# Kernel optimization log

Measured on AMD Instinct MI355X. Metric: run time of the kernel, lower is better.

Reference implementation:

```python
import jax, jax.numpy as jnp
import numpy as np

N_EMBD = 512
NUM_HEADS = 8
HEAD_SIZE = 64


def setup_inputs() -> dict:
    key = jax.random.key(0)
    ks = jax.random.split(key, 6)
    B, T, C, H, D = 64, 256, N_EMBD, NUM_HEADS, HEAD_SIZE
    s = 0.02
    return {
        "x": jax.random.normal(ks[0], (B, T, C), dtype=jnp.float32),
        "wq": jax.random.normal(ks[1], (H, C, D), dtype=jnp.float32) * s,
        "wk": jax.random.normal(ks[2], (H, C, D), dtype=jnp.float32) * s,
        "wv": jax.random.normal(ks[3], (H, C, D), dtype=jnp.float32) * s,
        "bq": jnp.zeros((H, D), dtype=jnp.float32),
        "bk": jnp.zeros((H, D), dtype=jnp.float32),
        "bv": jnp.zeros((H, D), dtype=jnp.float32),
        "wo": jax.random.normal(ks[4], (H * D, C), dtype=jnp.float32) * s,
        "bo": jnp.zeros((C,), dtype=jnp.float32),
    }


def reference(x, wq, wk, wv, bq, bk, bv, wo, bo):
    B, T, C = x.shape
    H, _, D = wq.shape
    # per-head QKV projections (vectorized over heads)
    q = jnp.einsum('btc,hcd->bhtd', x, wq) + bq[None, :, None, :]
    k = jnp.einsum('btc,hcd->bhtd', x, wk) + bk[None, :, None, :]
    v = jnp.einsum('btc,hcd->bhtd', x, wv) + bv[None, :, None, :]
    scale = 1.0 / jnp.sqrt(jnp.asarray(D, dtype=x.dtype))
    scores = jnp.einsum('bhtd,bhsd->bhts', q, k) * scale  # [B,H,T,T]
    causal = jnp.tril(jnp.ones((T, T), dtype=bool))
    scores = jnp.where(causal[None, None], scores, -jnp.inf)
    weights = jax.nn.softmax(scores, axis=-1)  # dropout omitted (eval mode)
    out = jnp.einsum('bhts,bhsd->bhtd', weights, v)  # [B,H,T,D]
    combined = out.transpose(0, 2, 1, 3).reshape(B, T, H * D)
    return combined @ wo + bo
```

## Files before the change

### kernel.cpp

```cpp
#include <hip/hip_runtime.h>

typedef unsigned int   u32;
typedef unsigned short u16;
typedef __attribute__((ext_vector_type(8))) short short8;
typedef __attribute__((ext_vector_type(4))) float f32x4;


__device__ __forceinline__ u16 f2bf(float f) {
    u32 u = __float_as_uint(f);
    u += 0x7fffu + ((u >> 16) & 1u);
    return (u16)(u >> 16);
}

__global__ void cast_x_kernel(const float* __restrict__ x, u16* __restrict__ xb) {
    int i = blockIdx.x * 256 + threadIdx.x;
    float4 v = ((const float4*)x)[i];
    ushort4 o;
    o.x = f2bf(v.x); o.y = f2bf(v.y); o.z = f2bf(v.z); o.w = f2bf(v.w);
    ((ushort4*)xb)[i] = o;
}

__global__ void pack_wqkv_kernel(const float* __restrict__ wq, const float* __restrict__ wk,
                                 const float* __restrict__ wv, u16* __restrict__ wt) {
    int i = blockIdx.x * 256 + threadIdx.x;
    int n = i >> 9, c = i & 511;
    int proj = n >> 9, hd = n & 511;
    int h = hd >> 6, d = hd & 63;
    const float* w = (proj == 0) ? wq : (proj == 1) ? wk : wv;
    wt[(size_t)n * 512 + c] = f2bf(w[h * 32768 + c * 64 + d]);
}

__global__ void pack_wo_kernel(const float* __restrict__ wo, u16* __restrict__ wt) {
    int i = blockIdx.x * 256 + threadIdx.x;
    int n = i >> 9, k = i & 511;
    wt[(size_t)n * 512 + k] = f2bf(wo[(size_t)k * 512 + n]);
}

template<int EPI>
__global__ __launch_bounds__(256)
void gemm128_kernel(const u16* __restrict__ A, const u16* __restrict__ Bt,
                    float* __restrict__ outf, const float* __restrict__ bo,
                    u16* __restrict__ Qb, u16* __restrict__ Kb, u16* __restrict__ Vb,
                    const float* __restrict__ bq, const float* __restrict__ bk,
                    const float* __restrict__ bv) {
    __shared__ __align__(16) u16 As[128 * 40];
    __shared__ __align__(16) u16 Bs[128 * 40];
    const int tid = threadIdx.x;
    const int m0 = blockIdx.y * 128;
    const int n0 = blockIdx.x * 128;
    const int r0 = tid >> 2;
    const int seg = tid & 3;
    const uint4* Ag = (const uint4*)(A + (size_t)m0 * 512);
    const uint4* Bg = (const uint4*)(Bt + (size_t)n0 * 512);
    uint4* AsV = (uint4*)As;
    uint4* BsV = (uint4*)Bs;

    uint4 a0 = Ag[r0 * 64 + seg], a1 = Ag[(r0 + 64) * 64 + seg];
    uint4 b0 = Bg[r0 * 64 + seg], b1 = Bg[(r0 + 64) * 64 + seg];

    const int w = tid >> 6, lane = tid & 63;
    const int wrow = (w >> 1) * 64, wcol = (w & 1) * 64;
    const int lm = lane & 15, quad = lane >> 4;

    f32x4 acc[4][4] = {};

    for (int kt = 0; kt < 16; ++kt) {
        __syncthreads();
        AsV[r0 * 5 + seg] = a0;  AsV[(r0 + 64) * 5 + seg] = a1;
        BsV[r0 * 5 + seg] = b0;  BsV[(r0 + 64) * 5 + seg] = b1;
        __syncthreads();
        if (kt < 15) {
            int ko = (kt + 1) * 4 + seg;
            a0 = Ag[r0 * 64 + ko]; a1 = Ag[(r0 + 64) * 64 + ko];
            b0 = Bg[r0 * 64 + ko]; b1 = Bg[(r0 + 64) * 64 + ko];
        }
        short8 af[4], bf[4];
        #pragma unroll
        for (int mi = 0; mi < 4; ++mi)
            af[mi] = *(const short8*)(As + (wrow + mi * 16 + lm) * 40 + quad * 8);
        #pragma unroll
        for (int ni = 0; ni < 4; ++ni)
            bf[ni] = *(const short8*)(Bs + (wcol + ni * 16 + lm) * 40 + quad * 8);
        #pragma unroll
        for (int mi = 0; mi < 4; ++mi)
            #pragma unroll
            for (int ni = 0; ni < 4; ++ni)
                acc[mi][ni] = __builtin_amdgcn_mfma_f32_16x16x32_bf16(af[mi], bf[ni], acc[mi][ni], 0, 0, 0);
    }

    if (EPI == 1) {
        #pragma unroll
        for (int ni = 0; ni < 4; ++ni) {
            int ncol = n0 + wcol + ni * 16 + lm;
            float bias = bo[ncol];
            #pragma unroll
            for (int mi = 0; mi < 4; ++mi) {
                int mbase = m0 + wrow + mi * 16 + quad * 4;
                #pragma unroll
                for (int r = 0; r < 4; ++r)
                    outf[(size_t)(mbase + r) * 512 + ncol] = acc[mi][ni][r] + bias;
            }
        }
    } else {
        #pragma unroll
        for (int ni = 0; ni < 4; ++ni) {
            int ncol = n0 + wcol + ni * 16 + lm;
            int proj = ncol >> 9, hd = ncol & 511;
            int h = hd >> 6, d = hd & 63;
            const float* bptr = (proj == 0) ? bq : (proj == 1) ? bk : bv;
            u16* dst = (proj == 0) ? Qb : (proj == 1) ? Kb : Vb;
            float bias = bptr[hd];
            #pragma unroll
            for (int mi = 0; mi < 4; ++mi) {
                int mbase = m0 + wrow + mi * 16 + quad * 4;
                #pragma unroll
                for (int r = 0; r < 4; ++r) {
                    int mrow = mbase + r;
                    int b = mrow >> 8, t = mrow & 255;
                    size_t idx = (proj == 2)
                        ? ((size_t)((b * 8 + h) * 64 + d) * 256 + t)
                        : ((size_t)((b * 8 + h) * 256 + t) * 64 + d);
                    dst[idx] = f2bf(acc[mi][ni][r] + bias);
                }
            }
        }
    }
}

__global__ __launch_bounds__(256)
void attn_mfma_kernel(const u16* __restrict__ Qg, const u16* __restrict__ Kg,
                      const u16* __restrict__ Vtg, u16* __restrict__ attn) {
    __shared__ __align__(16) u16 lds[36864];
    const int head = blockIdx.x;
    const int b = head >> 3, h = head & 7;
    const int tid = threadIdx.x;
    const size_t hb = (size_t)head * 16384;

    {
        const uint4* Ksrc = (const uint4*)(Kg + hb);
        const uint4* Vsrc = (const uint4*)(Vtg + hb);
        uint4* L4 = (uint4*)lds;
        #pragma unroll
        for (int it = 0; it < 8; ++it) {
            int g = it * 256 + tid;
            int kr = g >> 3, kc = g & 7;
            L4[kr * 8 + (kc ^ (kr & 7))] = Ksrc[g];
            int vr = g >> 5, vc = g & 31;
            L4[2048 + vr * 32 + (vc ^ (vr & 7))] = Vsrc[g];
        }
    }
    __syncthreads();

    const int w = tid >> 6, lane = tid & 63;
    const int lm = lane & 15, quad = lane >> 4;
    const int l7 = lm & 7;

    const int kx0 = (quad ^ l7) * 8;
    const int kx1 = ((4 + quad) ^ l7) * 8;
    const u16* Kbase = lds + lm * 64;
    const u16* Vbase = lds + 16384 + lm * 256;
    const int Pbase = 32768 + w * 1024;
    const int x0 = (lm >> 3) & 1;
    const int pw_even = Pbase + quad * 16 + l7 + x0 * 8;
    const int pw_odd  = Pbase + quad * 16 + l7 + (x0 ^ 1) * 8;
    const int pr0 = Pbase + ((lm & 3) * 4 + (quad >> 1)) * 64
                  + (2 * (lm >> 2) + ((quad & 1) ^ (lm & 1))) * 8;

    #pragma unroll 1
    for (int i = 0; i < 4; ++i) {
        const int t0 = i * 64 + w * 16;
        short8 qa0 = *(const short8*)(Qg + hb + (size_t)(t0 + lm) * 64 + quad * 8);
        short8 qa1 = *(const short8*)(Qg + hb + (size_t)(t0 + lm) * 64 + 32 + quad * 8);
        f32x4 O[4] = {};
        float mr[4] = {-INFINITY, -INFINITY, -INFINITY, -INFINITY};
        float lr[4] = {0.f, 0.f, 0.f, 0.f};

        #pragma unroll 1
        for (int j = 0; j <= i; ++j) {
            f32x4 S[4] = {};
            #pragma unroll
            for (int ni = 0; ni < 4; ++ni) {
                const u16* kp = Kbase + j * 4096 + ni * 1024;
                short8 kb0 = *(const short8*)(kp + kx0);
                short8 kb1 = *(const short8*)(kp + kx1);
                S[ni] = __builtin_amdgcn_mfma_f32_16x16x32_bf16(qa0, kb0, S[ni], 0, 0, 0);
                S[ni] = __builtin_amdgcn_mfma_f32_16x16x32_bf16(qa1, kb1, S[ni], 0, 0, 0);
            }
            if (j == i) {
                #pragma unroll
                for (int ni = 0; ni < 4; ++ni) {
                    int scol = ni * 16 + lm;
                    #pragma unroll
                    for (int rr = 0; rr < 4; ++rr) {
                        int tloc = w * 16 + quad * 4 + rr;
                        S[ni][rr] = (scol > tloc) ? -INFINITY : S[ni][rr] * 0.125f;
                    }
                }
            } else {
                #pragma unroll
                for (int ni = 0; ni < 4; ++ni)
                    #pragma unroll
                    for (int rr = 0; rr < 4; ++rr)
                        S[ni][rr] *= 0.125f;
            }
            float alpha[4];
            #pragma unroll
            for (int rr = 0; rr < 4; ++rr) {
                float mx = fmaxf(fmaxf(S[0][rr], S[1][rr]), fmaxf(S[2][rr], S[3][rr]));
                mx = fmaxf(mx, __shfl_xor(mx, 1));
                mx = fmaxf(mx, __shfl_xor(mx, 2));
                mx = fmaxf(mx, __shfl_xor(mx, 4));
                mx = fmaxf(mx, __shfl_xor(mx, 8));
                float mnew = fmaxf(mr[rr], mx);
                alpha[rr] = __expf(mr[rr] - mnew);
                mr[rr] = mnew;
            }
            __syncthreads();
            float rs[4] = {0.f, 0.f, 0.f, 0.f};
            #pragma unroll
            for (int ni = 0; ni < 4; ++ni) {
                #pragma unroll
                for (int rr = 0; rr < 4; ++rr) {
                    float p = __expf(S[ni][rr] - mr[rr]);
                    rs[rr] += p;
                    int addr = ((rr & 1) ? pw_odd : pw_even) + (rr * 4 + ni) * 64;
                    lds[addr] = f2bf(p);
                }
            }
            #pragma unroll
            for (int rr = 0; rr < 4; ++rr) {
                float s = rs[rr];
                s += __shfl_xor(s, 1);
                s += __shfl_xor(s, 2);
                s += __shfl_xor(s, 4);
                s += __shfl_xor(s, 8);
                lr[rr] = lr[rr] * alpha[rr] + s;
                O[0][rr] *= alpha[rr]; O[1][rr] *= alpha[rr];
                O[2][rr] *= alpha[rr]; O[3][rr] *= alpha[rr];
            }
            __syncthreads();
            short8 pa0 = *(const short8*)(lds + pr0);
            short8 pa1 = *(const short8*)(lds + pr0 + 128);
            #pragma unroll
            for (int nd = 0; nd < 4; ++nd) {
                const u16* vp = Vbase + nd * 4096 + j * 64;
                short8 vb0 = *(const short8*)(vp + kx0);
                short8 vb1 = *(const short8*)(vp + kx1);
                O[nd] = __builtin_amdgcn_mfma_f32_16x16x32_bf16(pa0, vb0, O[nd], 0, 0, 0);
                O[nd] = __builtin_amdgcn_mfma_f32_16x16x32_bf16(pa1, vb1, O[nd], 0, 0, 0);
            }
        }
        #pragma unroll
        for (int rr = 0; rr < 4; ++rr) {
            float inv = 1.0f / lr[rr];
            int t = t0 + quad * 4 + rr;
            u16* op = attn + (size_t)(b * 256 + t) * 512 + h * 64 + lm;
            op[0]  = f2bf(O[0][rr] * inv);
            op[16] = f2bf(O[1][rr] * inv);
            op[32] = f2bf(O[2][rr] * inv);
            op[48] = f2bf(O[3][rr] * inv);
        }
    }
}

extern "C" void kernel_launch(void* const* d_in, const int* in_sizes, int n_in,
                              void* d_out, int out_size, void* d_ws, size_t ws_size,
                              hipStream_t stream) {
    const float* x  = (const float*)d_in[0];
    const float* wq = (const float*)d_in[1];
    const float* wk = (const float*)d_in[2];
    const float* wv = (const float*)d_in[3];
    const float* bq = (const float*)d_in[4];
    const float* bk = (const float*)d_in[5];
    const float* bv = (const float*)d_in[6];
    const float* wo = (const float*)d_in[7];
    const float* bo = (const float*)d_in[8];
    float* out = (float*)d_out;

    char* ws = (char*)d_ws;
    const size_t SZ = 16777216;
    u16* xb    = (u16*)(ws);
    u16* Qb    = (u16*)(ws + SZ);
    u16* Kb    = (u16*)(ws + 2 * SZ);
    u16* Vt    = (u16*)(ws + 3 * SZ);
    u16* attn  = (u16*)(ws + 4 * SZ);
    u16* wqkvT = (u16*)(ws + 5 * SZ);
    u16* woT   = (u16*)(ws + 5 * SZ + 1572864);

    cast_x_kernel<<<8192, 256, 0, stream>>>(x, xb);
    pack_wqkv_kernel<<<3072, 256, 0, stream>>>(wq, wk, wv, wqkvT);
    pack_wo_kernel<<<1024, 256, 0, stream>>>(wo, woT);

    gemm128_kernel<0><<<dim3(12, 128), 256, 0, stream>>>(
        xb, wqkvT, nullptr, nullptr, Qb, Kb, Vt, bq, bk, bv);

    attn_mfma_kernel<<<512, 256, 0, stream>>>(Qb, Kb, Vt, attn);

    gemm128_kernel<1><<<dim3(4, 128), 256, 0, stream>>>(
        attn, woT, out, bo, nullptr, nullptr, nullptr, nullptr, nullptr, nullptr);
}
```

Measured before the change: 216.8 us.

## Split causal attention across two blocks per head and use direct global-to-LDS loads

The attention kernel now launches two blocks per head, each handling a balanced pair of causal query tiles, (0,3) or (1,2). This doubles the grid for better CU occupancy and load balance, at the cost of each block reloading the full K/V into LDS. The GEMM kernels replace the register-staged prefetch with global_load_lds builtins that write straight into unpadded LDS tiles. That removes VGPR staging but also removes the overlap of next-tile loads with MFMA work, and the unpadded stride may bring back LDS bank conflicts.

```diff
diff --git a/kernel.cpp b/kernel.cpp
--- a/kernel.cpp
+++ b/kernel.cpp
@@ -10,6 +10,12 @@
     u32 u = __float_as_uint(f);
     u += 0x7fffu + ((u >> 16) & 1u);
     return (u16)(u >> 16);
+}
+
+__device__ __forceinline__ void gload_lds16(const u16* g, u16* l) {
+    __builtin_amdgcn_global_load_lds(
+        (const __attribute__((address_space(1))) u32*)(const void*)g,
+        (__attribute__((address_space(3))) u32*)(void*)l, 16, 0, 0);
 }
 
 __global__ void cast_x_kernel(const float* __restrict__ x, u16* __restrict__ xb) {
@@ -43,20 +49,17 @@
                     u16* __restrict__ Qb, u16* __restrict__ Kb, u16* __restrict__ Vb,
                     const float* __restrict__ bq, const float* __restrict__ bk,
                     const float* __restrict__ bv) {
-    __shared__ __align__(16) u16 As[128 * 40];
-    __shared__ __align__(16) u16 Bs[128 * 40];
+    __shared__ __align__(16) u16 As[128 * 32];
+    __shared__ __align__(16) u16 Bs[128 * 32];
     const int tid = threadIdx.x;
     const int m0 = blockIdx.y * 128;
     const int n0 = blockIdx.x * 128;
-    const int r0 = tid >> 2;
-    const int seg = tid & 3;
-    const uint4* Ag = (const uint4*)(A + (size_t)m0 * 512);
-    const uint4* Bg = (const uint4*)(Bt + (size_t)n0 * 512);
-    uint4* AsV = (uint4*)As;
-    uint4* BsV = (uint4*)Bs;
-
-    uint4 a0 = Ag[r0 * 64 + seg], a1 = Ag[(r0 + 64) * 64 + seg];
-    uint4 b0 = Bg[r0 * 64 + seg], b1 = Bg[(r0 + 64) * 64 + seg];
+    const int lrow = tid >> 2;
+    const int seg  = tid & 3;
+    const u16* Ag = A  + (size_t)(m0 + lrow) * 512 + seg * 8;
+    const u16* Bg = Bt + (size_t)(n0 + lrow) * 512 + seg * 8;
+    u16* Asl = As + lrow * 32 + seg * 8;
+    u16* Bsl = Bs + lrow * 32 + seg * 8;
 
     const int w = tid >> 6, lane = tid & 63;
     const int wrow = (w >> 1) * 64, wcol = (w & 1) * 64;
@@ -66,21 +69,18 @@
 
     for (int kt = 0; kt < 16; ++kt) {
         __syncthreads();
-        AsV[r0 * 5 + seg] = a0;  AsV[(r0 + 64) * 5 + seg] = a1;
-        BsV[r0 * 5 + seg] = b0;  BsV[(r0 + 64) * 5 + seg] = b1;
+        gload_lds16(Ag + kt * 32,             Asl);
+        gload_lds16(Ag + 64 * 512 + kt * 32,  Asl + 64 * 32);
+        gload_lds16(Bg + kt * 32,             Bsl);
+        gload_lds16(Bg + 64 * 512 + kt * 32,  Bsl + 64 * 32);
         __syncthreads();
-        if (kt < 15) {
-            int ko = (kt + 1) * 4 + seg;
-            a0 = Ag[r0 * 64 + ko]; a1 = Ag[(r0 + 64) * 64 + ko];
-            b0 = Bg[r0 * 64 + ko]; b1 = Bg[(r0 + 64) * 64 + ko];
-        }
         short8 af[4], bf[4];
         #pragma unroll
         for (int mi = 0; mi < 4; ++mi)
-            af[mi] = *(const short8*)(As + (wrow + mi * 16 + lm) * 40 + quad * 8);
+            af[mi] = *(const short8*)(As + (wrow + mi * 16 + lm) * 32 + quad * 8);
         #pragma unroll
         for (int ni = 0; ni < 4; ++ni)
-            bf[ni] = *(const short8*)(Bs + (wcol + ni * 16 + lm) * 40 + quad * 8);
+            bf[ni] = *(const short8*)(Bs + (wcol + ni * 16 + lm) * 32 + quad * 8);
         #pragma unroll
         for (int mi = 0; mi < 4; ++mi)
             #pragma unroll
@@ -131,7 +131,8 @@
 void attn_mfma_kernel(const u16* __restrict__ Qg, const u16* __restrict__ Kg,
                       const u16* __restrict__ Vtg, u16* __restrict__ attn) {
     __shared__ __align__(16) u16 lds[36864];
-    const int head = blockIdx.x;
+    const int head = blockIdx.x >> 1;
+    const int iset = blockIdx.x & 1;
     const int b = head >> 3, h = head & 7;
     const int tid = threadIdx.x;
     const size_t hb = (size_t)head * 16384;
@@ -167,7 +168,8 @@
                   + (2 * (lm >> 2) + ((quad & 1) ^ (lm & 1))) * 8;
 
     #pragma unroll 1
-    for (int i = 0; i < 4; ++i) {
+    for (int ii = 0; ii < 2; ++ii) {
+        const int i = iset ? (ii ? 2 : 1) : (ii ? 3 : 0);
         const int t0 = i * 64 + w * 16;
         short8 qa0 = *(const short8*)(Qg + hb + (size_t)(t0 + lm) * 64 + quad * 8);
         short8 qa1 = *(const short8*)(Qg + hb + (size_t)(t0 + lm) * 64 + 32 + quad * 8);
@@ -294,7 +296,7 @@
     gemm128_kernel<0><<<dim3(12, 128), 256, 0, stream>>>(
         xb, wqkvT, nullptr, nullptr, Qb, Kb, Vt, bq, bk, bv);
 
-    attn_mfma_kernel<<<512, 256, 0, stream>>>(Qb, Kb, Vt, attn);
+    attn_mfma_kernel<<<1024, 256, 0, stream>>>(Qb, Kb, Vt, attn);
 
     gemm128_kernel<1><<<dim3(4, 128), 256, 0, stream>>>(
         attn, woT, out, bo, nullptr, nullptr, nullptr, nullptr, nullptr, nullptr);
```

New measurement: 219.1 us. Within noise of the previous version (+1.1%).
